# Optimization experiments

Hardware: AMD Instinct MI355X
Metric: run time of the kernel (lower is better)

## Reference

```python
import jax, jax.numpy as jnp
import numpy as np
from jax import lax

KERNEL = 21
SHIFT = KERNEL - 1  # 20
NUM_LEVELS = 2
EPS = 1e-5
NEG_SLOPE = 0.01


def _conv1d(x, w):
    # x: [B, Cin, T], w: [Cout, Cin, K] -> [B, Cout, T-K+1]
    return lax.conv_general_dilated(x, w, window_strides=(1,), padding='VALID',
                                    dimension_numbers=('NCH', 'OIH', 'NCH'))


def _batchnorm_train(x, gamma, beta):
    # training-mode BN over (N, L) per channel, biased variance (torch semantics)
    mean = jnp.mean(x, axis=(0, 2), keepdims=True)
    var = jnp.mean((x - mean) ** 2, axis=(0, 2), keepdims=True)
    return (x - mean) * lax.rsqrt(var + EPS) * gamma[None, :, None] + beta[None, :, None]


def _spp(y, L, num_levels, pool):
    # y: [B, C, Tc]; L: [B] valid lengths. Level i has 2^i bins:
    #   bin j covers [j*floor(L/2^i), j*floor(L/2^i)+ceil(L/2^i)), matching
    #   F.max_pool1d/avg_pool1d(kernel=ceil(f), stride=floor(f)) on x[:, :, :L].
    B, C, Tc = y.shape
    pos = jnp.arange(Tc)[None, :]                     # [1, Tc]
    Lf = L.astype(jnp.float32)
    outs = []
    for i in range(num_levels):
        k = 2 ** i
        f = Lf / k
        stride = jnp.floor(f).astype(jnp.int32)        # [B]
        kern = jnp.ceil(f).astype(jnp.int32)           # [B]
        bins = []
        for j in range(k):
            start = j * stride                         # [B]
            mask = (pos >= start[:, None]) & (pos < (start + kern)[:, None])  # [B, Tc]
            m = mask[:, None, :]                       # [B, 1, Tc]
            if pool == 'max':
                bins.append(jnp.max(jnp.where(m, y, -jnp.inf), axis=-1))      # [B, C]
            else:
                s = jnp.sum(jnp.where(m, y, jnp.zeros((), y.dtype)), axis=-1)
                bins.append(s / kern[:, None].astype(y.dtype))
        # torch .view flattens (C, k) channel-major
        outs.append(jnp.stack(bins, axis=-1).reshape(B, C * k))
    return jnp.concatenate(outs, axis=1)               # [B, C*(2^n - 1)]


def setup_inputs() -> dict:
    key = jax.random.key(0)
    k1, k2, k3, k4, k5 = jax.random.split(key, 5)
    B, C, T = 32, 64, 16384
    n_tasks = 2
    n_lin = 2 * C * (2 ** NUM_LEVELS - 1)  # 384
    x = jax.random.normal(k1, (B, C, T), dtype=jnp.float32)
    orig_len = jax.random.randint(k2, (B,), T // 2, T + 1, dtype=jnp.int32)
    w1 = jax.random.normal(k3, (C, C, KERNEL), dtype=jnp.float32) * 0.05
    w2 = jax.random.normal(k4, (C, C, KERNEL), dtype=jnp.float32) * 0.05
    g1 = jnp.ones((C,), jnp.float32); b1 = jnp.zeros((C,), jnp.float32)
    g2 = jnp.ones((C,), jnp.float32); b2 = jnp.zeros((C,), jnp.float32)
    fc_w = jax.random.normal(k5, (n_tasks, n_lin), dtype=jnp.float32) * 0.05
    fc_b = jnp.zeros((n_tasks,), jnp.float32)
    return {"x": x, "orig_len": orig_len, "w1": w1, "g1": g1, "b1": b1,
            "w2": w2, "g2": g2, "b2": b2, "fc_w": fc_w, "fc_b": fc_b}


def reference(x, orig_len, w1, g1, b1, w2, g2, b2, fc_w, fc_b):
    L = orig_len - SHIFT  # valid conv-output length per sample
    y1 = jax.nn.leaky_relu(_batchnorm_train(_conv1d(x, w1), g1, b1), NEG_SLOPE)
    p1 = _spp(y1, L, NUM_LEVELS, 'max')
    y2 = jax.nn.leaky_relu(_batchnorm_train(_conv1d(x, w2), g2, b2), NEG_SLOPE)
    p2 = _spp(y2, L, NUM_LEVELS, 'avg')
    feat = jnp.concatenate([p1, p2], axis=1)           # [B, 384]
    return feat @ fc_w.T + fc_b
```

## Files before the change

### kernel.cpp

```cpp
#include <hip/hip_runtime.h>

#define AS1 __attribute__((address_space(1)))
#define AS3 __attribute__((address_space(3)))

using u16 = unsigned short;
using u32 = unsigned int;
typedef __attribute__((ext_vector_type(8))) short bf16x8;
typedef __attribute__((ext_vector_type(4))) float f32x4;

constexpr int Bn    = 32;
constexpr int Tn    = 16384;
constexpr int TCn   = 16364;
constexpr int TILE  = 256;
constexpr int XROWS = 280;
constexpr int TPAD  = 16416;

__device__ __forceinline__ u16 f2bf(float f) {
  union { float f; u32 u; } v; v.f = f;
  u32 u = v.u;
  u += 0x7fffu + ((u >> 16) & 1u);
  return (u16)(u >> 16);
}
__device__ __forceinline__ float bf2f(u32 h) {
  union { u32 u; float f; } v; v.u = h << 16; return v.f;
}
__device__ __forceinline__ u32 encf(float f) {
  union { float f; u32 u; } v; v.f = f;
  return (v.u & 0x80000000u) ? ~v.u : (v.u | 0x80000000u);
}
__device__ __forceinline__ float decf(u32 u) {
  union { u32 u; float f; } v;
  v.u = (u & 0x80000000u) ? (u ^ 0x80000000u) : ~u;
  return v.f;
}
__device__ __forceinline__ void gload_lds16(const void* g, void* l) {
  __builtin_amdgcn_global_load_lds((const AS1 u32*)g, (AS3 u32*)l, 16, 0, 0);
}
__device__ __forceinline__ float leaky(float z) { return z > 0.f ? z : 0.01f * z; }

__global__ __launch_bounds__(256) void transpose_x(const float* __restrict__ x,
                                                   u16* __restrict__ x_t,
                                                   const float* __restrict__ w1,
                                                   const float* __restrict__ w2,
                                                   u16* __restrict__ wf1,
                                                   u16* __restrict__ wf2) {
  __shared__ u16 lt[64][64];
  const int bx  = blockIdx.x;
  const int tid = threadIdx.x;

  if (bx >= Bn * 256) {
    const int bxx = bx - Bn * 256;
    const int cv  = bxx / 42;
    const int c   = bxx % 42;
    const float* w = cv ? w2 : w1;
    u16* wf = cv ? wf2 : wf1;
    const int ct   = tid >> 6;
    const int lane = tid & 63;
    const int q  = lane >> 4;
    const int rr = lane & 15;
    const int k  = c >> 1;
    const int cb = (c & 1) * 32;
    const int co = ct * 16 + rr;
    u16 us[8] __attribute__((aligned(16)));
#pragma unroll
    for (int j = 0; j < 8; ++j) {
      int ci = cb + q * 8 + j;
      us[j] = f2bf(w[((size_t)co * 64 + ci) * 21 + k]);
    }
    *(uint4*)&wf[((size_t)(c * 4 + ct) * 64 + lane) * 8] = *(const uint4*)us;
    return;
  }

  const int b   = bx >> 8;
  const int tt  = bx & 255;
  const int t0  = tt * 64;
  const int ci0 = (tid & 15) * 4;
  const int tl0 = (tid >> 4) * 4;
  float4 v[4];
#pragma unroll
  for (int j = 0; j < 4; ++j)
    v[j] = *(const float4*)(x + (size_t)(b * 64 + ci0 + j) * Tn + t0 + tl0);
  float vr[4][4] = {{v[0].x,v[0].y,v[0].z,v[0].w},{v[1].x,v[1].y,v[1].z,v[1].w},
                    {v[2].x,v[2].y,v[2].z,v[2].w},{v[3].x,v[3].y,v[3].z,v[3].w}};
#pragma unroll
  for (int e = 0; e < 4; ++e) {
    int tl = tl0 + e;
    u32 lo = (u32)f2bf(vr[0][e]) | ((u32)f2bf(vr[1][e]) << 16);
    u32 hi = (u32)f2bf(vr[2][e]) | ((u32)f2bf(vr[3][e]) << 16);
    uint2 pk = make_uint2(lo, hi);
    *(uint2*)&lt[tl][ci0] = pk;
  }
  __syncthreads();
  const int row = tid >> 2;
  const int seg = tid & 3;
  const int c0  = seg * 16;
  const int sw  = (row & 7) * 8;
  u16* op = x_t + ((size_t)b * TPAD + t0 + row) * 64 + c0;
  *(uint4*)op       = *(const uint4*)&lt[row][c0 ^ sw];
  *(uint4*)(op + 8) = *(const uint4*)&lt[row][(c0 + 8) ^ sw];
  if (tt == 0) {
    uint4 z = make_uint4(0u, 0u, 0u, 0u);
    uint4* pz = (uint4*)(x_t + ((size_t)b * TPAD + Tn) * 64);
    pz[tid] = z;
  }
}

__global__ __launch_bounds__(256, 2) void conv_mfma(const u16* __restrict__ x_t,
                                                    const u16* __restrict__ wf1,
                                                    const u16* __restrict__ wf2,
                                                    u16* __restrict__ y1,
                                                    u16* __restrict__ y2,
                                                    float* __restrict__ stats) {
  __shared__ u16 xs[XROWS * 64];
  __shared__ u16 wsw[7 * 4 * 64 * 8];
  __shared__ float sred[128];

  const int bid  = blockIdx.x;
  const int cv   = bid & 1;
  const int tmp  = bid >> 1;
  const int tile = tmp & 63;
  const int b    = tmp >> 6;
  const int t0   = tile * TILE;
  const int tid  = threadIdx.x;
  const int w    = tid >> 6;
  const int lane = tid & 63;
  const int q    = lane >> 4;
  const int r    = lane & 15;
  const u16* wf  = cv ? wf2 : wf1;

  if (tid < 128) sred[tid] = 0.f;

  const u16* xg = x_t + ((size_t)b * TPAD + t0) * 64;
  for (int s = w; s < 35; s += 4)
    gload_lds16(xg + (size_t)s * 512 + lane * 8, &xs[s * 512]);

  f32x4 acc[4][4];
#pragma unroll
  for (int a = 0; a < 4; ++a)
#pragma unroll
    for (int t = 0; t < 4; ++t)
      acc[a][t] = (f32x4){0.f, 0.f, 0.f, 0.f};

  for (int g = 0; g < 6; ++g) {
    const u16* wg = wf + (size_t)g * 14336;
    for (int s = w; s < 28; s += 4)
      gload_lds16(wg + (size_t)s * 512 + lane * 8, &wsw[s * 512]);
    __syncthreads();
#pragma unroll
    for (int cl = 0; cl < 7; ++cl) {
      const int c  = g * 7 + cl;
      const int k  = c >> 1;
      const int cb = (c & 1) * 32;
      bf16x8 af[4];
#pragma unroll
      for (int ct = 0; ct < 4; ++ct)
        af[ct] = *(const bf16x8*)&wsw[((cl * 4 + ct) * 64 + lane) * 8];
      bf16x8 bx[4];
#pragma unroll
      for (int tt = 0; tt < 4; ++tt) {
        int p = w * 64 + tt * 16 + r + k;
        int cidx = (cb + q * 8) ^ ((p & 7) * 8);
        bx[tt] = *(const bf16x8*)&xs[p * 64 + cidx];
      }
#pragma unroll
      for (int ct = 0; ct < 4; ++ct)
#pragma unroll
        for (int tt = 0; tt < 4; ++tt)
          acc[ct][tt] = __builtin_amdgcn_mfma_f32_16x16x32_bf16(af[ct], bx[tt], acc[ct][tt], 0, 0, 0);
    }
    __syncthreads();
  }

#pragma unroll
  for (int ct = 0; ct < 4; ++ct)
#pragma unroll
    for (int i = 0; i < 4; ++i) {
      float sv = 0.f, sq = 0.f;
#pragma unroll
      for (int tt = 0; tt < 4; ++tt) {
        int tg = t0 + w * 64 + tt * 16 + r;
        if (tg < TCn) {
          float v = acc[ct][tt][i];
          sv += v; sq += v * v;
        }
      }
#pragma unroll
      for (int m = 1; m < 16; m <<= 1) {
        sv += __shfl_xor(sv, m, 64);
        sq += __shfl_xor(sq, m, 64);
      }
      if (r == 0) {
        int co = ct * 16 + q * 4 + i;
        atomicAdd(&sred[co * 2], sv);
        atomicAdd(&sred[co * 2 + 1], sq);
      }
    }

  u16* ys = xs;
#pragma unroll
  for (int ct = 0; ct < 4; ++ct)
#pragma unroll
    for (int tt = 0; tt < 4; ++tt) {
      int tl = w * 64 + tt * 16 + r;
#pragma unroll
      for (int i = 0; i < 4; ++i) {
        int co = ct * 16 + q * 4 + i;
        ys[tl * 64 + co] = f2bf(acc[ct][tt][i]);
      }
    }
  __syncthreads();
  u16* yo = (cv ? y2 : y1) + ((size_t)b * Tn + t0) * 64;
#pragma unroll
  for (int m = 0; m < 8; ++m) {
    int idx = (m * 256 + tid) * 8;
    *(uint4*)(yo + idx) = *(const uint4*)(ys + idx);
  }
  if (tid < 128) atomicAdd(&stats[cv * 128 + tid], sred[tid]);
}

__global__ __launch_bounds__(256) void spp(const u16* __restrict__ y1,
                                           const u16* __restrict__ y2,
                                           const float* __restrict__ stats,
                                           const float* __restrict__ g1v,
                                           const float* __restrict__ b1v,
                                           const float* __restrict__ g2v,
                                           const float* __restrict__ b2v,
                                           const int* __restrict__ orig_len,
                                           u32* __restrict__ featU) {
  const int bx = blockIdx.x;
  const int b  = bx >> 4;
  const int ch = bx & 15;
  const int tid  = threadIdx.x;
  const int g    = tid & 15;
  const int trow = tid >> 4;
  const int co0  = g * 4;
  const int L     = orig_len[b] - 20;
  const int str2  = L >> 1;
  const int kern2 = L - str2;
  const float Nf = 32.0f * 16364.0f;
  float a1[4], c1[4], a2[4], c2[4];
#pragma unroll
  for (int j = 0; j < 4; ++j) {
    int co = co0 + j;
    float s, sq, mean, var;
    s = stats[co * 2]; sq = stats[co * 2 + 1];
    mean = s / Nf; var = sq / Nf - mean * mean; if (var < 0.f) var = 0.f;
    a1[j] = g1v[co] * rsqrtf(var + 1e-5f);
    c1[j] = b1v[co] - mean * a1[j];
    s = stats[128 + co * 2]; sq = stats[128 + co * 2 + 1];
    mean = s / Nf; var = sq / Nf - mean * mean; if (var < 0.f) var = 0.f;
    a2[j] = g2v[co] * rsqrtf(var + 1e-5f);
    c2[j] = b2v[co] - mean * a2[j];
  }
  float m1[4] = {-3.4e38f,-3.4e38f,-3.4e38f,-3.4e38f};
  float m2[4] = {-3.4e38f,-3.4e38f,-3.4e38f,-3.4e38f};
  float s0[4] = {0,0,0,0}, sb0[4] = {0,0,0,0}, sb1[4] = {0,0,0,0};
  const int tbase = ch * 1024;
  int tend = tbase + 1024;
  if (tend > L) tend = L;
  const u16* p1 = y1 + (size_t)b * Tn * 64 + co0;
  const u16* p2 = y2 + (size_t)b * Tn * 64 + co0;
  for (int t = tbase + trow; t < tend; t += 16) {
    uint2 v1 = *(const uint2*)(p1 + (size_t)t * 64);
    uint2 v2 = *(const uint2*)(p2 + (size_t)t * 64);
    float f1[4] = { bf2f(v1.x & 0xffffu), bf2f(v1.x >> 16),
                    bf2f(v1.y & 0xffffu), bf2f(v1.y >> 16) };
    float f2[4] = { bf2f(v2.x & 0xffffu), bf2f(v2.x >> 16),
                    bf2f(v2.y & 0xffffu), bf2f(v2.y >> 16) };
    bool in0 = (t < kern2), in1 = (t >= str2);
#pragma unroll
    for (int j = 0; j < 4; ++j) {
      float z1 = leaky(fmaf(a1[j], f1[j], c1[j]));
      float z2 = leaky(fmaf(a2[j], f2[j], c2[j]));
      s0[j] += z2;
      if (in0) { m1[j] = fmaxf(m1[j], z1); sb0[j] += z2; }
      if (in1) { m2[j] = fmaxf(m2[j], z1); sb1[j] += z2; }
    }
  }
#pragma unroll
  for (int m = 16; m <= 32; m <<= 1) {
#pragma unroll
    for (int j = 0; j < 4; ++j) {
      m1[j]  = fmaxf(m1[j], __shfl_xor(m1[j], m, 64));
      m2[j]  = fmaxf(m2[j], __shfl_xor(m2[j], m, 64));
      s0[j]  += __shfl_xor(s0[j],  m, 64);
      sb0[j] += __shfl_xor(sb0[j], m, 64);
      sb1[j] += __shfl_xor(sb1[j], m, 64);
    }
  }
  if (((tid & 63) >> 4) == 0) {
    u32* fb = featU + (size_t)b * 384;
    float* ff = (float*)fb;
#pragma unroll
    for (int j = 0; j < 4; ++j) {
      int co = co0 + j;
      u32 e1 = encf(m1[j]), e2 = encf(m2[j]);
      atomicMax(&fb[co], e1 > e2 ? e1 : e2);
      atomicMax(&fb[64 + co * 2], e1);
      atomicMax(&fb[64 + co * 2 + 1], e2);
      atomicAdd(&ff[192 + co], s0[j]);
      atomicAdd(&ff[256 + co * 2], sb0[j]);
      atomicAdd(&ff[256 + co * 2 + 1], sb1[j]);
    }
  }
}

__global__ void fc(const u32* __restrict__ featU,
                   const int* __restrict__ orig_len,
                   const float* __restrict__ fc_w,
                   const float* __restrict__ fc_b,
                   float* __restrict__ out) {
  const int tid  = threadIdx.x;
  const int pair = tid >> 2;
  const int part = tid & 3;
  const int b = pair >> 1;
  const int n = pair & 1;
  const int L = orig_len[b] - 20;
  const int kern2 = L - (L >> 1);
  const u32* fb = featU + (size_t)b * 384;
  const float* ff = (const float*)fb;
  float acc = 0.f;
  for (int j = part; j < 384; j += 4) {
    float fv;
    if (j < 192)      fv = decf(fb[j]);
    else if (j < 256) fv = ff[j] / (float)L;
    else              fv = ff[j] / (float)kern2;
    acc += fv * fc_w[n * 384 + j];
  }
  acc += __shfl_xor(acc, 1, 64);
  acc += __shfl_xor(acc, 2, 64);
  if (part == 0) out[b * 2 + n] = acc + fc_b[n];
}

extern "C" void kernel_launch(void* const* d_in, const int* in_sizes, int n_in,
                              void* d_out, int out_size, void* d_ws, size_t ws_size,
                              hipStream_t stream) {
  const float* x        = (const float*)d_in[0];
  const int*   orig_len = (const int*)d_in[1];
  const float* w1  = (const float*)d_in[2];
  const float* g1  = (const float*)d_in[3];
  const float* b1  = (const float*)d_in[4];
  const float* w2  = (const float*)d_in[5];
  const float* g2  = (const float*)d_in[6];
  const float* b2  = (const float*)d_in[7];
  const float* fcw = (const float*)d_in[8];
  const float* fcb = (const float*)d_in[9];
  float* out = (float*)d_out;

  char* ws = (char*)d_ws;
  const size_t XT_BYTES = (size_t)Bn * TPAD * 64 * 2;
  const size_t Y_BYTES  = (size_t)Bn * Tn * 64 * 2;
  const size_t WF_BYTES = (size_t)42 * 4 * 64 * 8 * 2;
  size_t off = 0;
  u16* x_t = (u16*)(ws + off); off += XT_BYTES;
  u16* y1  = (u16*)(ws + off); off += Y_BYTES;
  u16* y2  = (u16*)(ws + off); off += Y_BYTES;
  u16* wf1 = (u16*)(ws + off); off += WF_BYTES;
  u16* wf2 = (u16*)(ws + off); off += WF_BYTES;
  float* stats = (float*)(ws + off);
  u32*   featU = (u32*)(ws + off + 1024);
  const size_t SMALL_BYTES = 1024 + 49152;

  hipMemsetAsync(ws + off, 0, SMALL_BYTES, stream);
  transpose_x<<<Bn * 256 + 84, 256, 0, stream>>>(x, x_t, w1, w2, wf1, wf2);
  conv_mfma<<<Bn * 64 * 2, 256, 0, stream>>>(x_t, wf1, wf2, y1, y2, stats);
  spp<<<Bn * 16, 256, 0, stream>>>(y1, y2, stats, g1, b1, g2, b2, orig_len, featU);
  fc<<<1, 256, 0, stream>>>(featU, orig_len, fcw, fcb, out);
  (void)in_sizes; (void)n_in; (void)out_size; (void)ws_size;
}
```

Baseline: 483.6 us.

## Triple-buffer conv weight staging, widen spp grid, parallelize fc per batch

The conv kernel now streams weights in 21 small chunks through a three-slot LDS ring. It waits with explicit vmcnt and raw barriers instead of reloading a large chunk behind two __syncthreads per group, and raises wave priority around the MFMA burst. The BN stats reduction skips bounds checks on full tiles. The spp kernel is split into four times as many blocks with an unrolled inner loop, and fc runs one block per batch with a full wave reduction. Together these aim to hide weight-load latency and improve occupancy of the reduction kernels. In exchange there are more barriers per tile and more atomics in spp.

```diff
diff --git a/kernel.cpp b/kernel.cpp
--- a/kernel.cpp
+++ b/kernel.cpp
@@ -112,7 +112,7 @@
                                                     u16* __restrict__ y2,
                                                     float* __restrict__ stats) {
   __shared__ u16 xs[XROWS * 64];
-  __shared__ u16 wsw[7 * 4 * 64 * 8];
+  __shared__ u16 wsw[3][4096];
   __shared__ float sred[128];
 
   const int bid  = blockIdx.x;
@@ -129,10 +129,19 @@
   const u16* wf  = cv ? wf2 : wf1;
 
   if (tid < 128) sred[tid] = 0.f;
+  __syncthreads();
+
+  auto stage_w = [&](int m, int gg) {
+    const u16* wg = wf + (size_t)gg * 4096;
+    gload_lds16(wg + (size_t)w * 512 + lane * 8,       &wsw[m][w * 512]);
+    gload_lds16(wg + (size_t)(w + 4) * 512 + lane * 8, &wsw[m][(w + 4) * 512]);
+  };
 
   const u16* xg = x_t + ((size_t)b * TPAD + t0) * 64;
   for (int s = w; s < 35; s += 4)
     gload_lds16(xg + (size_t)s * 512 + lane * 8, &xs[s * 512]);
+  stage_w(0, 0);
+  stage_w(1, 1);
 
   f32x4 acc[4][4];
 #pragma unroll
@@ -141,20 +150,23 @@
     for (int t = 0; t < 4; ++t)
       acc[a][t] = (f32x4){0.f, 0.f, 0.f, 0.f};
 
-  for (int g = 0; g < 6; ++g) {
-    const u16* wg = wf + (size_t)g * 14336;
-    for (int s = w; s < 28; s += 4)
-      gload_lds16(wg + (size_t)s * 512 + lane * 8, &wsw[s * 512]);
-    __syncthreads();
-#pragma unroll
-    for (int cl = 0; cl < 7; ++cl) {
-      const int c  = g * 7 + cl;
+  int mc = 0;
+  int ms = 2;
+  for (int g = 0; g < 21; ++g) {
+    if (g < 20) asm volatile("s_waitcnt vmcnt(2)" ::: "memory");
+    else        asm volatile("s_waitcnt vmcnt(0)" ::: "memory");
+    __builtin_amdgcn_s_barrier();
+    if (g < 19) stage_w(ms, g + 2);
+
+#pragma unroll
+    for (int cl = 0; cl < 2; ++cl) {
+      const int c  = g * 2 + cl;
       const int k  = c >> 1;
       const int cb = (c & 1) * 32;
       bf16x8 af[4];
 #pragma unroll
       for (int ct = 0; ct < 4; ++ct)
-        af[ct] = *(const bf16x8*)&wsw[((cl * 4 + ct) * 64 + lane) * 8];
+        af[ct] = *(const bf16x8*)&wsw[mc][((cl * 4 + ct) * 64 + lane) * 8];
       bf16x8 bx[4];
 #pragma unroll
       for (int tt = 0; tt < 4; ++tt) {
@@ -162,26 +174,38 @@
         int cidx = (cb + q * 8) ^ ((p & 7) * 8);
         bx[tt] = *(const bf16x8*)&xs[p * 64 + cidx];
       }
+      __builtin_amdgcn_s_setprio(1);
 #pragma unroll
       for (int ct = 0; ct < 4; ++ct)
 #pragma unroll
         for (int tt = 0; tt < 4; ++tt)
           acc[ct][tt] = __builtin_amdgcn_mfma_f32_16x16x32_bf16(af[ct], bx[tt], acc[ct][tt], 0, 0, 0);
-    }
-    __syncthreads();
-  }
-
+      __builtin_amdgcn_s_setprio(0);
+    }
+    mc = (mc == 2) ? 0 : mc + 1;
+    ms = (ms == 2) ? 0 : ms + 1;
+  }
+
+  const bool full = (t0 + TILE <= TCn);
 #pragma unroll
   for (int ct = 0; ct < 4; ++ct)
 #pragma unroll
     for (int i = 0; i < 4; ++i) {
       float sv = 0.f, sq = 0.f;
-#pragma unroll
-      for (int tt = 0; tt < 4; ++tt) {
-        int tg = t0 + w * 64 + tt * 16 + r;
-        if (tg < TCn) {
+      if (full) {
+#pragma unroll
+        for (int tt = 0; tt < 4; ++tt) {
           float v = acc[ct][tt][i];
           sv += v; sq += v * v;
+        }
+      } else {
+#pragma unroll
+        for (int tt = 0; tt < 4; ++tt) {
+          int tg = t0 + w * 64 + tt * 16 + r;
+          if (tg < TCn) {
+            float v = acc[ct][tt][i];
+            sv += v; sq += v * v;
+          }
         }
       }
 #pragma unroll
@@ -195,6 +219,8 @@
         atomicAdd(&sred[co * 2 + 1], sq);
       }
     }
+
+  __syncthreads();
 
   u16* ys = xs;
 #pragma unroll
@@ -228,8 +254,8 @@
                                            const int* __restrict__ orig_len,
                                            u32* __restrict__ featU) {
   const int bx = blockIdx.x;
-  const int b  = bx >> 4;
-  const int ch = bx & 15;
+  const int b  = bx >> 6;
+  const int ch = bx & 63;
   const int tid  = threadIdx.x;
   const int g    = tid & 15;
   const int trow = tid >> 4;
@@ -255,12 +281,13 @@
   float m1[4] = {-3.4e38f,-3.4e38f,-3.4e38f,-3.4e38f};
   float m2[4] = {-3.4e38f,-3.4e38f,-3.4e38f,-3.4e38f};
   float s0[4] = {0,0,0,0}, sb0[4] = {0,0,0,0}, sb1[4] = {0,0,0,0};
-  const int tbase = ch * 1024;
-  int tend = tbase + 1024;
+  const int tbase = ch * 256;
+  int tend = tbase + 256;
   if (tend > L) tend = L;
   const u16* p1 = y1 + (size_t)b * Tn * 64 + co0;
   const u16* p2 = y2 + (size_t)b * Tn * 64 + co0;
-  for (int t = tbase + trow; t < tend; t += 16) {
+
+  auto body = [&](int t) {
     uint2 v1 = *(const uint2*)(p1 + (size_t)t * 64);
     uint2 v2 = *(const uint2*)(p2 + (size_t)t * 64);
     float f1[4] = { bf2f(v1.x & 0xffffu), bf2f(v1.x >> 16),
@@ -276,7 +303,19 @@
       if (in0) { m1[j] = fmaxf(m1[j], z1); sb0[j] += z2; }
       if (in1) { m2[j] = fmaxf(m2[j], z1); sb1[j] += z2; }
     }
-  }
+  };
+
+  if (tend == tbase + 256) {
+    for (int it = 0; it < 16; it += 4) {
+#pragma unroll
+      for (int u = 0; u < 4; ++u)
+        body(tbase + trow + (it + u) * 16);
+    }
+  } else {
+    for (int t = tbase + trow; t < tend; t += 16)
+      body(t);
+  }
+
 #pragma unroll
   for (int m = 16; m <= 32; m <<= 1) {
 #pragma unroll
@@ -305,31 +344,32 @@
   }
 }
 
-__global__ void fc(const u32* __restrict__ featU,
-                   const int* __restrict__ orig_len,
-                   const float* __restrict__ fc_w,
-                   const float* __restrict__ fc_b,
-                   float* __restrict__ out) {
+__global__ __launch_bounds__(128) void fc(const u32* __restrict__ featU,
+                                          const int* __restrict__ orig_len,
+                                          const float* __restrict__ fc_w,
+                                          const float* __restrict__ fc_b,
+                                          float* __restrict__ out) {
+  const int b    = blockIdx.x;
   const int tid  = threadIdx.x;
-  const int pair = tid >> 2;
-  const int part = tid & 3;
-  const int b = pair >> 1;
-  const int n = pair & 1;
+  const int n    = tid >> 6;
+  const int lane = tid & 63;
   const int L = orig_len[b] - 20;
   const int kern2 = L - (L >> 1);
   const u32* fb = featU + (size_t)b * 384;
   const float* ff = (const float*)fb;
   float acc = 0.f;
-  for (int j = part; j < 384; j += 4) {
+#pragma unroll
+  for (int jj = 0; jj < 6; ++jj) {
+    int j = jj * 64 + lane;
     float fv;
     if (j < 192)      fv = decf(fb[j]);
     else if (j < 256) fv = ff[j] / (float)L;
     else              fv = ff[j] / (float)kern2;
     acc += fv * fc_w[n * 384 + j];
   }
-  acc += __shfl_xor(acc, 1, 64);
-  acc += __shfl_xor(acc, 2, 64);
-  if (part == 0) out[b * 2 + n] = acc + fc_b[n];
+#pragma unroll
+  for (int m = 1; m < 64; m <<= 1) acc += __shfl_xor(acc, m, 64);
+  if (lane == 0) out[b * 2 + n] = acc + fc_b[n];
 }
 
 extern "C" void kernel_launch(void* const* d_in, const int* in_sizes, int n_in,
@@ -364,7 +404,7 @@
   hipMemsetAsync(ws + off, 0, SMALL_BYTES, stream);
   transpose_x<<<Bn * 256 + 84, 256, 0, stream>>>(x, x_t, w1, w2, wf1, wf2);
   conv_mfma<<<Bn * 64 * 2, 256, 0, stream>>>(x_t, wf1, wf2, y1, y2, stats);
-  spp<<<Bn * 16, 256, 0, stream>>>(y1, y2, stats, g1, b1, g2, b2, orig_len, featU);
-  fc<<<1, 256, 0, stream>>>(featU, orig_len, fcw, fcb, out);
+  spp<<<Bn * 64, 256, 0, stream>>>(y1, y2, stats, g1, b1, g2, b2, orig_len, featU);
+  fc<<<Bn, 128, 0, stream>>>(featU, orig_len, fcw, fcb, out);
   (void)in_sizes; (void)n_in; (void)out_size; (void)ws_size;
 }
```

After: 591.7 us. +22.4%, slower.
